# Kernel tuning notes

Hardware: AMD Instinct MI355X
Metric: run time of the kernel (lower is better)

## Reference

```python
import jax, jax.numpy as jnp
import numpy as np

N = 50000
E = 800000
IN_C = 128
HID = 16
HEADS = 8
OUT_C = 64
NEG_SLOPE = 0.2


def setup_inputs() -> dict:
    key = jax.random.key(0)
    ks = jax.random.split(key, 12)
    x = jax.random.normal(ks[0], (N, IN_C), dtype=jnp.float32)
    edge_index = jax.random.randint(ks[1], (2, E), 0, N, dtype=jnp.int32)
    s = 0.1
    W1 = jax.random.normal(ks[2], (IN_C, HEADS * HID), dtype=jnp.float32) * s
    a1_src = jax.random.normal(ks[3], (HEADS, HID), dtype=jnp.float32) * s
    a1_dst = jax.random.normal(ks[4], (HEADS, HID), dtype=jnp.float32) * s
    b1 = jnp.zeros((HEADS * HID,), dtype=jnp.float32)
    W2 = jax.random.normal(ks[5], (HEADS * HID, OUT_C), dtype=jnp.float32) * s
    a2_src = jax.random.normal(ks[6], (1, OUT_C), dtype=jnp.float32) * s
    a2_dst = jax.random.normal(ks[7], (1, OUT_C), dtype=jnp.float32) * s
    b2 = jnp.zeros((OUT_C,), dtype=jnp.float32)
    return {"x": x, "edge_index": edge_index, "W1": W1, "a1_src": a1_src,
            "a1_dst": a1_dst, "b1": b1, "W2": W2, "a2_src": a2_src,
            "a2_dst": a2_dst, "b2": b2}


def gat_conv(x, src, dst, W, a_src, a_dst, b, heads, ch):
    # linear projection -> [N, H, C]
    h = (x @ W).reshape(N, heads, ch)
    # per-node attention logits [N, H]
    al_s = jnp.einsum('nhc,hc->nh', h, a_src)
    al_d = jnp.einsum('nhc,hc->nh', h, a_dst)
    # per-edge logits [E, H]
    e = jax.nn.leaky_relu(al_s[src] + al_d[dst], NEG_SLOPE)
    # segment softmax over incoming edges of each dst node
    emax = jax.ops.segment_max(e, dst, num_segments=N)
    ee = jnp.exp(e - emax[dst])
    denom = jax.ops.segment_sum(ee, dst, num_segments=N)
    alpha = ee / (denom[dst] + 1e-16)
    # weighted scatter-aggregate of source messages
    msg = h[src] * alpha[:, :, None]  # [E, H, C]
    out = jax.ops.segment_sum(msg, dst, num_segments=N)
    return out.reshape(N, heads * ch) + b


def reference(x, edge_index, W1, a1_src, a1_dst, b1, W2, a2_src, a2_dst, b2):
    # add self loops (PyG GATConv default add_self_loops=True)
    loops = jnp.arange(N, dtype=edge_index.dtype)
    src = jnp.concatenate([edge_index[0], loops])
    dst = jnp.concatenate([edge_index[1], loops])
    h = gat_conv(x, src, dst, W1, a1_src, a1_dst, b1, HEADS, HID)
    h = jax.nn.relu(h)
    # dropout p=0.6 is identity in eval mode
    out = gat_conv(h, src, dst, W2, a2_src, a2_dst, b2, 1, OUT_C)
    return out
```

## Files before the change

kernel.cpp:

```cpp
#include <hip/hip_runtime.h>
#include <hip/hip_fp16.h>
#include <math.h>

#define N_NODES 50000
#define E_EDGES 800000
#define IN_C    128
#define HID     16
#define HEADS   8
#define OUT_C   64
#define NEG_SLOPE 0.2f
#define ELLW    64

template <int OUTC, int HEADS_T>
__global__ __launch_bounds__(256) void fused_gemm_fill(
    const float* __restrict__ X, const float* __restrict__ W, __half* __restrict__ H,
    const float* __restrict__ a_src, const float* __restrict__ a_dst,
    float* __restrict__ als, float* __restrict__ ald, int nrows,
    const int* __restrict__ src, const int* __restrict__ dst,
    int* __restrict__ cursor, int* __restrict__ ell) {
    constexpr int CPG = OUTC / 4;
    constexpr int RT = (256 / CPG) * 4;
    constexpr int GROUP = (OUTC / HEADS_T) / 4;
    __shared__ __half wsh[IN_C * OUTC];
    __shared__ float xs[RT * 132];
    const int bid = blockIdx.x;

    if (bid & 1) {
        const int tid = (bid >> 1) * 256 + threadIdx.x;
        if (tid < E_EDGES / 4) {
            const int4 s4 = ((const int4*)src)[tid];
            const int4 d4 = ((const int4*)dst)[tid];
            const int p0 = atomicAdd(&cursor[d4.x], 1);
            const int p1 = atomicAdd(&cursor[d4.y], 1);
            const int p2 = atomicAdd(&cursor[d4.z], 1);
            const int p3 = atomicAdd(&cursor[d4.w], 1);
            ell[(size_t)d4.x * ELLW + p0] = s4.x;
            ell[(size_t)d4.y * ELLW + p1] = s4.y;
            ell[(size_t)d4.z * ELLW + p2] = s4.z;
            ell[(size_t)d4.w * ELLW + p3] = s4.w;
        }
        return;
    }

    const int t = threadIdx.x;
    for (int f = t * 4; f < IN_C * OUTC; f += 1024) {
        const float4 w4 = *(const float4*)&W[f];
        *(__half2*)&wsh[f]     = __float22half2_rn(make_float2(w4.x, w4.y));
        *(__half2*)&wsh[f + 2] = __float22half2_rn(make_float2(w4.z, w4.w));
    }
    const int row0 = (bid >> 1) * 64;
    const int cp = t % CPG;
    const int r0 = (t / CPG) * 4;
    float asr[4], adr[4];
#pragma unroll
    for (int j = 0; j < 4; ++j) {
        asr[j] = a_src[cp * 4 + j];
        adr[j] = a_dst[cp * 4 + j];
    }
    for (int rb = 0; rb < 64; rb += RT) {
        __syncthreads();
        for (int f = t * 4; f < RT * IN_C; f += 1024) {
            const int r = f >> 7, k = f & 127;
            int rl = row0 + rb + r;
            if (rl >= nrows) rl = nrows - 1;
            *(float4*)&xs[r * 132 + k] = *(const float4*)&X[(size_t)rl * IN_C + k];
        }
        __syncthreads();
        float acc[4][4] = {};
#pragma unroll 8
        for (int k = 0; k < IN_C; ++k) {
            const float2 wlo = __half22float2(*(const __half2*)&wsh[k * OUTC + cp * 4]);
            const float2 whi = __half22float2(*(const __half2*)&wsh[k * OUTC + cp * 4 + 2]);
#pragma unroll
            for (int i = 0; i < 4; ++i) {
                const float xi = xs[(r0 + i) * 132 + k];
                acc[i][0] += xi * wlo.x;
                acc[i][1] += xi * wlo.y;
                acc[i][2] += xi * whi.x;
                acc[i][3] += xi * whi.y;
            }
        }
#pragma unroll
        for (int i = 0; i < 4; ++i) {
            const int r = row0 + rb + r0 + i;
            float ps = acc[i][0] * asr[0] + acc[i][1] * asr[1] +
                       acc[i][2] * asr[2] + acc[i][3] * asr[3];
            float pd = acc[i][0] * adr[0] + acc[i][1] * adr[1] +
                       acc[i][2] * adr[2] + acc[i][3] * adr[3];
#pragma unroll
            for (int off = 1; off < GROUP; off <<= 1) {
                ps += __shfl_xor(ps, off);
                pd += __shfl_xor(pd, off);
            }
            if (r < nrows) {
                __half* hp = H + (size_t)r * OUTC + cp * 4;
                *(__half2*)(hp)     = __float22half2_rn(make_float2(acc[i][0], acc[i][1]));
                *(__half2*)(hp + 2) = __float22half2_rn(make_float2(acc[i][2], acc[i][3]));
                if ((cp % GROUP) == 0) {
                    const int hd = cp / GROUP;
                    als[(size_t)r * HEADS_T + hd] = ps;
                    ald[(size_t)r * HEADS_T + hd] = pd;
                }
            }
        }
    }
}

template <int OUTC, int HEADS_T>
__global__ __launch_bounds__(256) void gemm_tiled(const float* __restrict__ X,
                                                  const float* __restrict__ W,
                                                  __half* __restrict__ H,
                                                  const float* __restrict__ a_src,
                                                  const float* __restrict__ a_dst,
                                                  float* __restrict__ als,
                                                  float* __restrict__ ald, int nrows) {
    constexpr int CPG = OUTC / 4;
    constexpr int RT = (256 / CPG) * 4;
    constexpr int GROUP = (OUTC / HEADS_T) / 4;
    __shared__ __half wsh[IN_C * OUTC];
    __shared__ float xs[RT * 132];
    const int t = threadIdx.x;
    for (int f = t * 4; f < IN_C * OUTC; f += 1024) {
        const float4 w4 = *(const float4*)&W[f];
        *(__half2*)&wsh[f]     = __float22half2_rn(make_float2(w4.x, w4.y));
        *(__half2*)&wsh[f + 2] = __float22half2_rn(make_float2(w4.z, w4.w));
    }
    const int row0 = blockIdx.x * 64;
    const int cp = t % CPG;
    const int r0 = (t / CPG) * 4;
    float asr[4], adr[4];
#pragma unroll
    for (int j = 0; j < 4; ++j) {
        asr[j] = a_src[cp * 4 + j];
        adr[j] = a_dst[cp * 4 + j];
    }
    for (int rb = 0; rb < 64; rb += RT) {
        __syncthreads();
        for (int f = t * 4; f < RT * IN_C; f += 1024) {
            const int r = f >> 7, k = f & 127;
            int rl = row0 + rb + r;
            if (rl >= nrows) rl = nrows - 1;
            *(float4*)&xs[r * 132 + k] = *(const float4*)&X[(size_t)rl * IN_C + k];
        }
        __syncthreads();
        float acc[4][4] = {};
#pragma unroll 8
        for (int k = 0; k < IN_C; ++k) {
            const float2 wlo = __half22float2(*(const __half2*)&wsh[k * OUTC + cp * 4]);
            const float2 whi = __half22float2(*(const __half2*)&wsh[k * OUTC + cp * 4 + 2]);
#pragma unroll
            for (int i = 0; i < 4; ++i) {
                const float xi = xs[(r0 + i) * 132 + k];
                acc[i][0] += xi * wlo.x;
                acc[i][1] += xi * wlo.y;
                acc[i][2] += xi * whi.x;
                acc[i][3] += xi * whi.y;
            }
        }
#pragma unroll
        for (int i = 0; i < 4; ++i) {
            const int r = row0 + rb + r0 + i;
            float ps = acc[i][0] * asr[0] + acc[i][1] * asr[1] +
                       acc[i][2] * asr[2] + acc[i][3] * asr[3];
            float pd = acc[i][0] * adr[0] + acc[i][1] * adr[1] +
                       acc[i][2] * adr[2] + acc[i][3] * adr[3];
#pragma unroll
            for (int off = 1; off < GROUP; off <<= 1) {
                ps += __shfl_xor(ps, off);
                pd += __shfl_xor(pd, off);
            }
            if (r < nrows) {
                __half* hp = H + (size_t)r * OUTC + cp * 4;
                *(__half2*)(hp)     = __float22half2_rn(make_float2(acc[i][0], acc[i][1]));
                *(__half2*)(hp + 2) = __float22half2_rn(make_float2(acc[i][2], acc[i][3]));
                if ((cp % GROUP) == 0) {
                    const int hd = cp / GROUP;
                    als[(size_t)r * HEADS_T + hd] = ps;
                    ald[(size_t)r * HEADS_T + hd] = pd;
                }
            }
        }
    }
}

__device__ __forceinline__ float lrelu_exp(float v) {
    v = v > 0.f ? v : NEG_SLOPE * v;
    return __expf(v);
}

__global__ void agg1(const int* __restrict__ cnt, const int* __restrict__ ell,
                     const float* __restrict__ als, const float* __restrict__ ald,
                     const __half* __restrict__ H, const float* __restrict__ b,
                     float* __restrict__ out) {
    int i = blockIdx.x * blockDim.x + threadIdx.x;
    if (i >= N_NODES * 32) return;
    const int n = i >> 5, t = i & 31, h = t >> 2, cg = t & 3;
    const int deg = cnt[n];
    const int* ep = ell + (size_t)n * ELLW;
    const float ad = ald[n * HEADS + h];
    float ssum;
    float4 acc;
    {
        const float w = lrelu_exp(als[n * HEADS + h] + ad);
        const __half2* hp = (const __half2*)(H + ((size_t)n * HEADS + h) * HID + cg * 4);
        const float2 a0 = __half22float2(hp[0]);
        const float2 a1 = __half22float2(hp[1]);
        ssum = w;
        acc = make_float4(w * a0.x, w * a0.y, w * a1.x, w * a1.y);
    }
    int p = 0;
    for (; p + 4 <= deg; p += 4) {
        const int4 s4 = *(const int4*)(ep + p);
        const float v0 = als[s4.x * HEADS + h];
        const float v1 = als[s4.y * HEADS + h];
        const float v2 = als[s4.z * HEADS + h];
        const float v3 = als[s4.w * HEADS + h];
        const __half2* h0 = (const __half2*)(H + ((size_t)s4.x * HEADS + h) * HID + cg * 4);
        const __half2* h1 = (const __half2*)(H + ((size_t)s4.y * HEADS + h) * HID + cg * 4);
        const __half2* h2 = (const __half2*)(H + ((size_t)s4.z * HEADS + h) * HID + cg * 4);
        const __half2* h3 = (const __half2*)(H + ((size_t)s4.w * HEADS + h) * HID + cg * 4);
        const __half2 m00 = h0[0], m01 = h0[1];
        const __half2 m10 = h1[0], m11 = h1[1];
        const __half2 m20 = h2[0], m21 = h2[1];
        const __half2 m30 = h3[0], m31 = h3[1];
        const float w0 = lrelu_exp(v0 + ad);
        const float w1 = lrelu_exp(v1 + ad);
        const float w2 = lrelu_exp(v2 + ad);
        const float w3 = lrelu_exp(v3 + ad);
        ssum += (w0 + w1) + (w2 + w3);
        float2 f;
        f = __half22float2(m00); acc.x += w0 * f.x; acc.y += w0 * f.y;
        f = __half22float2(m01); acc.z += w0 * f.x; acc.w += w0 * f.y;
        f = __half22float2(m10); acc.x += w1 * f.x; acc.y += w1 * f.y;
        f = __half22float2(m11); acc.z += w1 * f.x; acc.w += w1 * f.y;
        f = __half22float2(m20); acc.x += w2 * f.x; acc.y += w2 * f.y;
        f = __half22float2(m21); acc.z += w2 * f.x; acc.w += w2 * f.y;
        f = __half22float2(m30); acc.x += w3 * f.x; acc.y += w3 * f.y;
        f = __half22float2(m31); acc.z += w3 * f.x; acc.w += w3 * f.y;
    }
    for (; p < deg; ++p) {
        const int s = ep[p];
        const float w = lrelu_exp(als[s * HEADS + h] + ad);
        const __half2* hp = (const __half2*)(H + ((size_t)s * HEADS + h) * HID + cg * 4);
        const float2 a0 = __half22float2(hp[0]);
        const float2 a1 = __half22float2(hp[1]);
        ssum += w;
        acc.x += w * a0.x; acc.y += w * a0.y; acc.z += w * a1.x; acc.w += w * a1.y;
    }
    const float inv = 1.f / (ssum + 1e-16f);
    const int c0 = h * HID + cg * 4;
    float4 r;
    r.x = acc.x * inv + b[c0 + 0];
    r.y = acc.y * inv + b[c0 + 1];
    r.z = acc.z * inv + b[c0 + 2];
    r.w = acc.w * inv + b[c0 + 3];
    r.x = r.x > 0.f ? r.x : 0.f;
    r.y = r.y > 0.f ? r.y : 0.f;
    r.z = r.z > 0.f ? r.z : 0.f;
    r.w = r.w > 0.f ? r.w : 0.f;
    *(float4*)(out + (size_t)n * IN_C + c0) = r;
}

__global__ void agg2(const int* __restrict__ cnt, const int* __restrict__ ell,
                     const float* __restrict__ als, const float* __restrict__ ald,
                     const __half* __restrict__ H, const float* __restrict__ b,
                     float* __restrict__ out) {
    int i = blockIdx.x * blockDim.x + threadIdx.x;
    if (i >= N_NODES * 16) return;
    const int n = i >> 4, cg = i & 15;
    const int deg = cnt[n];
    const int* ep = ell + (size_t)n * ELLW;
    const float ad = ald[n];
    float ssum;
    float4 acc;
    {
        const float w = lrelu_exp(als[n] + ad);
        const __half2* hp = (const __half2*)(H + (size_t)n * OUT_C + cg * 4);
        const float2 a0 = __half22float2(hp[0]);
        const float2 a1 = __half22float2(hp[1]);
        ssum = w;
        acc = make_float4(w * a0.x, w * a0.y, w * a1.x, w * a1.y);
    }
    int p = 0;
    for (; p + 4 <= deg; p += 4) {
        const int4 s4 = *(const int4*)(ep + p);
        const float v0 = als[s4.x];
        const float v1 = als[s4.y];
        const float v2 = als[s4.z];
        const float v3 = als[s4.w];
        const __half2* h0 = (const __half2*)(H + (size_t)s4.x * OUT_C + cg * 4);
        const __half2* h1 = (const __half2*)(H + (size_t)s4.y * OUT_C + cg * 4);
        const __half2* h2 = (const __half2*)(H + (size_t)s4.z * OUT_C + cg * 4);
        const __half2* h3 = (const __half2*)(H + (size_t)s4.w * OUT_C + cg * 4);
        const __half2 m00 = h0[0], m01 = h0[1];
        const __half2 m10 = h1[0], m11 = h1[1];
        const __half2 m20 = h2[0], m21 = h2[1];
        const __half2 m30 = h3[0], m31 = h3[1];
        const float w0 = lrelu_exp(v0 + ad);
        const float w1 = lrelu_exp(v1 + ad);
        const float w2 = lrelu_exp(v2 + ad);
        const float w3 = lrelu_exp(v3 + ad);
        ssum += (w0 + w1) + (w2 + w3);
        float2 f;
        f = __half22float2(m00); acc.x += w0 * f.x; acc.y += w0 * f.y;
        f = __half22float2(m01); acc.z += w0 * f.x; acc.w += w0 * f.y;
        f = __half22float2(m10); acc.x += w1 * f.x; acc.y += w1 * f.y;
        f = __half22float2(m11); acc.z += w1 * f.x; acc.w += w1 * f.y;
        f = __half22float2(m20); acc.x += w2 * f.x; acc.y += w2 * f.y;
        f = __half22float2(m21); acc.z += w2 * f.x; acc.w += w2 * f.y;
        f = __half22float2(m30); acc.x += w3 * f.x; acc.y += w3 * f.y;
        f = __half22float2(m31); acc.z += w3 * f.x; acc.w += w3 * f.y;
    }
    for (; p < deg; ++p) {
        const int s = ep[p];
        const float w = lrelu_exp(als[s] + ad);
        const __half2* hp = (const __half2*)(H + (size_t)s * OUT_C + cg * 4);
        const float2 a0 = __half22float2(hp[0]);
        const float2 a1 = __half22float2(hp[1]);
        ssum += w;
        acc.x += w * a0.x; acc.y += w * a0.y; acc.z += w * a1.x; acc.w += w * a1.y;
    }
    const float inv = 1.f / (ssum + 1e-16f);
    const int c0 = cg * 4;
    float4 r;
    r.x = acc.x * inv + b[c0 + 0];
    r.y = acc.y * inv + b[c0 + 1];
    r.z = acc.z * inv + b[c0 + 2];
    r.w = acc.w * inv + b[c0 + 3];
    *(float4*)(out + (size_t)n * OUT_C + c0) = r;
}

extern "C" void kernel_launch(void* const* d_in, const int* in_sizes, int n_in,
                              void* d_out, int out_size, void* d_ws, size_t ws_size,
                              hipStream_t stream) {
    const float* x      = (const float*)d_in[0];
    const int*   ei     = (const int*)d_in[1];
    const float* W1     = (const float*)d_in[2];
    const float* a1_src = (const float*)d_in[3];
    const float* a1_dst = (const float*)d_in[4];
    const float* b1     = (const float*)d_in[5];
    const float* W2     = (const float*)d_in[6];
    const float* a2_src = (const float*)d_in[7];
    const float* a2_dst = (const float*)d_in[8];
    const float* b2     = (const float*)d_in[9];
    const int* src = ei;
    const int* dst = ei + E_EDGES;
    float* outp = (float*)d_out;

    char* wsb = (char*)d_ws;
    float*  acc1 = (float*)wsb;
    __half* h1   = (__half*)(acc1 + (size_t)N_NODES * IN_C);
    __half* h2   = h1 + (size_t)N_NODES * IN_C;
    float*  als1 = (float*)(h2 + (size_t)N_NODES * OUT_C);
    float*  ald1 = als1 + N_NODES * HEADS;
    float*  als2 = ald1 + N_NODES * HEADS;
    float*  ald2 = als2 + N_NODES;
    int*    cursor = (int*)(ald2 + N_NODES);
    int*    ell    = cursor + N_NODES;

    hipMemsetAsync(cursor, 0, N_NODES * sizeof(int), stream);

    {
        const int gemm_blocks = (N_NODES + 63) / 64;
        const int fill_blocks = (E_EDGES / 4 + 255) / 256;
        (void)fill_blocks;
        fused_gemm_fill<IN_C, HEADS><<<gemm_blocks * 2, 256, 0, stream>>>(
            x, W1, h1, a1_src, a1_dst, als1, ald1, N_NODES, src, dst, cursor, ell);
    }
    {
        int n = N_NODES * 32;
        agg1<<<(n + 255) / 256, 256, 0, stream>>>(cursor, ell, als1, ald1, h1, b1, acc1);
    }

    gemm_tiled<OUT_C, 1><<<(N_NODES + 63) / 64, 256, 0, stream>>>(
        acc1, W2, h2, a2_src, a2_dst, als2, ald2, N_NODES);
    {
        int n = N_NODES * 16;
        agg2<<<(n + 255) / 256, 256, 0, stream>>>(cursor, ell, als2, ald2, h2, b2, outp);
    }
}
```

Baseline: 233.0 us.

## Fuse layer-1 aggregation with layer-2 projection GEMM

Merges the first-layer attention aggregation and the second-layer linear projection into one kernel. Each block aggregates 8 nodes, keeps the ReLU'd 128-wide rows in shared memory and multiplies them by W2 (staged as fp16 in LDS), writing h2 and the layer-2 attention logits directly. This removes the fp32 intermediate buffer round-trip through global memory and one kernel launch. In exchange, every block of 8 nodes reloads and converts the whole 16 KB W2 into shared memory, and the 32 KB LDS footprint per block may limit occupancy of the latency-bound gather loop.

```diff
diff --git a/kernel.cpp b/kernel.cpp
--- a/kernel.cpp
+++ b/kernel.cpp
@@ -106,95 +106,29 @@
     }
 }
 
-template <int OUTC, int HEADS_T>
-__global__ __launch_bounds__(256) void gemm_tiled(const float* __restrict__ X,
-                                                  const float* __restrict__ W,
-                                                  __half* __restrict__ H,
-                                                  const float* __restrict__ a_src,
-                                                  const float* __restrict__ a_dst,
-                                                  float* __restrict__ als,
-                                                  float* __restrict__ ald, int nrows) {
-    constexpr int CPG = OUTC / 4;
-    constexpr int RT = (256 / CPG) * 4;
-    constexpr int GROUP = (OUTC / HEADS_T) / 4;
-    __shared__ __half wsh[IN_C * OUTC];
-    __shared__ float xs[RT * 132];
-    const int t = threadIdx.x;
-    for (int f = t * 4; f < IN_C * OUTC; f += 1024) {
-        const float4 w4 = *(const float4*)&W[f];
-        *(__half2*)&wsh[f]     = __float22half2_rn(make_float2(w4.x, w4.y));
-        *(__half2*)&wsh[f + 2] = __float22half2_rn(make_float2(w4.z, w4.w));
-    }
-    const int row0 = blockIdx.x * 64;
-    const int cp = t % CPG;
-    const int r0 = (t / CPG) * 4;
-    float asr[4], adr[4];
-#pragma unroll
-    for (int j = 0; j < 4; ++j) {
-        asr[j] = a_src[cp * 4 + j];
-        adr[j] = a_dst[cp * 4 + j];
-    }
-    for (int rb = 0; rb < 64; rb += RT) {
-        __syncthreads();
-        for (int f = t * 4; f < RT * IN_C; f += 1024) {
-            const int r = f >> 7, k = f & 127;
-            int rl = row0 + rb + r;
-            if (rl >= nrows) rl = nrows - 1;
-            *(float4*)&xs[r * 132 + k] = *(const float4*)&X[(size_t)rl * IN_C + k];
-        }
-        __syncthreads();
-        float acc[4][4] = {};
-#pragma unroll 8
-        for (int k = 0; k < IN_C; ++k) {
-            const float2 wlo = __half22float2(*(const __half2*)&wsh[k * OUTC + cp * 4]);
-            const float2 whi = __half22float2(*(const __half2*)&wsh[k * OUTC + cp * 4 + 2]);
-#pragma unroll
-            for (int i = 0; i < 4; ++i) {
-                const float xi = xs[(r0 + i) * 132 + k];
-                acc[i][0] += xi * wlo.x;
-                acc[i][1] += xi * wlo.y;
-                acc[i][2] += xi * whi.x;
-                acc[i][3] += xi * whi.y;
-            }
-        }
-#pragma unroll
-        for (int i = 0; i < 4; ++i) {
-            const int r = row0 + rb + r0 + i;
-            float ps = acc[i][0] * asr[0] + acc[i][1] * asr[1] +
-                       acc[i][2] * asr[2] + acc[i][3] * asr[3];
-            float pd = acc[i][0] * adr[0] + acc[i][1] * adr[1] +
-                       acc[i][2] * adr[2] + acc[i][3] * adr[3];
-#pragma unroll
-            for (int off = 1; off < GROUP; off <<= 1) {
-                ps += __shfl_xor(ps, off);
-                pd += __shfl_xor(pd, off);
-            }
-            if (r < nrows) {
-                __half* hp = H + (size_t)r * OUTC + cp * 4;
-                *(__half2*)(hp)     = __float22half2_rn(make_float2(acc[i][0], acc[i][1]));
-                *(__half2*)(hp + 2) = __float22half2_rn(make_float2(acc[i][2], acc[i][3]));
-                if ((cp % GROUP) == 0) {
-                    const int hd = cp / GROUP;
-                    als[(size_t)r * HEADS_T + hd] = ps;
-                    ald[(size_t)r * HEADS_T + hd] = pd;
-                }
-            }
-        }
-    }
-}
-
 __device__ __forceinline__ float lrelu_exp(float v) {
     v = v > 0.f ? v : NEG_SLOPE * v;
     return __expf(v);
 }
 
-__global__ void agg1(const int* __restrict__ cnt, const int* __restrict__ ell,
-                     const float* __restrict__ als, const float* __restrict__ ald,
-                     const __half* __restrict__ H, const float* __restrict__ b,
-                     float* __restrict__ out) {
-    int i = blockIdx.x * blockDim.x + threadIdx.x;
-    if (i >= N_NODES * 32) return;
-    const int n = i >> 5, t = i & 31, h = t >> 2, cg = t & 3;
+__global__ __launch_bounds__(256) void agg1_gemm2(
+    const int* __restrict__ cnt, const int* __restrict__ ell,
+    const float* __restrict__ als, const float* __restrict__ ald,
+    const __half* __restrict__ H, const float* __restrict__ b,
+    const float* __restrict__ W2, const float* __restrict__ a2_src,
+    const float* __restrict__ a2_dst, __half* __restrict__ H2,
+    float* __restrict__ als2, float* __restrict__ ald2) {
+    __shared__ __half wsh[IN_C * OUT_C];
+    __shared__ float xrow[8 * 132];
+    const int t = threadIdx.x;
+    for (int f = t * 4; f < IN_C * OUT_C; f += 1024) {
+        const float4 w4 = *(const float4*)&W2[f];
+        *(__half2*)&wsh[f]     = __float22half2_rn(make_float2(w4.x, w4.y));
+        *(__half2*)&wsh[f + 2] = __float22half2_rn(make_float2(w4.z, w4.w));
+    }
+
+    const int nl = t >> 5, tl = t & 31, h = tl >> 2, cg = tl & 3;
+    const int n = blockIdx.x * 8 + nl;
     const int deg = cnt[n];
     const int* ep = ell + (size_t)n * ELLW;
     const float ad = ald[n * HEADS + h];
@@ -258,7 +192,40 @@
     r.y = r.y > 0.f ? r.y : 0.f;
     r.z = r.z > 0.f ? r.z : 0.f;
     r.w = r.w > 0.f ? r.w : 0.f;
-    *(float4*)(out + (size_t)n * IN_C + c0) = r;
+    float* xr = &xrow[nl * 132 + c0];
+    xr[0] = r.x; xr[1] = r.y; xr[2] = r.z; xr[3] = r.w;
+
+    __syncthreads();
+
+    const int j0 = (t & 31) * 2;
+    const int ng = t >> 5;
+    const int n2 = blockIdx.x * 8 + ng;
+    const float a2s0 = a2_src[j0], a2s1 = a2_src[j0 + 1];
+    const float a2d0 = a2_dst[j0], a2d1 = a2_dst[j0 + 1];
+    float o0 = 0.f, o1 = 0.f;
+    const float* xb = &xrow[ng * 132];
+#pragma unroll 4
+    for (int c = 0; c < IN_C; c += 4) {
+        const float4 xv = *(const float4*)&xb[c];
+        const float2 wa = __half22float2(*(const __half2*)&wsh[(c + 0) * OUT_C + j0]);
+        const float2 wb = __half22float2(*(const __half2*)&wsh[(c + 1) * OUT_C + j0]);
+        const float2 wc = __half22float2(*(const __half2*)&wsh[(c + 2) * OUT_C + j0]);
+        const float2 wd = __half22float2(*(const __half2*)&wsh[(c + 3) * OUT_C + j0]);
+        o0 += xv.x * wa.x + xv.y * wb.x + xv.z * wc.x + xv.w * wd.x;
+        o1 += xv.x * wa.y + xv.y * wb.y + xv.z * wc.y + xv.w * wd.y;
+    }
+    float ps = o0 * a2s0 + o1 * a2s1;
+    float pd = o0 * a2d0 + o1 * a2d1;
+#pragma unroll
+    for (int off = 1; off < 32; off <<= 1) {
+        ps += __shfl_xor(ps, off);
+        pd += __shfl_xor(pd, off);
+    }
+    *(__half2*)(H2 + (size_t)n2 * OUT_C + j0) = __float22half2_rn(make_float2(o0, o1));
+    if ((t & 31) == 0) {
+        als2[n2] = ps;
+        ald2[n2] = pd;
+    }
 }
 
 __global__ void agg2(const int* __restrict__ cnt, const int* __restrict__ ell,
@@ -348,8 +315,7 @@
     float* outp = (float*)d_out;
 
     char* wsb = (char*)d_ws;
-    float*  acc1 = (float*)wsb;
-    __half* h1   = (__half*)(acc1 + (size_t)N_NODES * IN_C);
+    __half* h1   = (__half*)wsb;
     __half* h2   = h1 + (size_t)N_NODES * IN_C;
     float*  als1 = (float*)(h2 + (size_t)N_NODES * OUT_C);
     float*  ald1 = als1 + N_NODES * HEADS;
@@ -362,18 +328,13 @@
 
     {
         const int gemm_blocks = (N_NODES + 63) / 64;
-        const int fill_blocks = (E_EDGES / 4 + 255) / 256;
-        (void)fill_blocks;
         fused_gemm_fill<IN_C, HEADS><<<gemm_blocks * 2, 256, 0, stream>>>(
             x, W1, h1, a1_src, a1_dst, als1, ald1, N_NODES, src, dst, cursor, ell);
     }
-    {
-        int n = N_NODES * 32;
-        agg1<<<(n + 255) / 256, 256, 0, stream>>>(cursor, ell, als1, ald1, h1, b1, acc1);
-    }
-
-    gemm_tiled<OUT_C, 1><<<(N_NODES + 63) / 64, 256, 0, stream>>>(
-        acc1, W2, h2, a2_src, a2_dst, als2, ald2, N_NODES);
+
+    agg1_gemm2<<<N_NODES / 8, 256, 0, stream>>>(
+        cursor, ell, als1, ald1, h1, b1, W2, a2_src, a2_dst, h2, als2, ald2);
+
     {
         int n = N_NODES * 16;
         agg2<<<(n + 255) / 256, 256, 0, stream>>>(cursor, ell, als2, ald2, h2, b2, outp);
```

Result: no change. 230.6 us (-1.0%).
